# Performance work log

Hardware: AMD Instinct MI355X
Metric: run time of the kernel (lower is better)

## Reference

```python
import jax, jax.numpy as jnp
import numpy as np

N = 40000      # input points
M = 40000      # output points
E = 500000     # flat neighbor edges (ragged flattened)
F = 32         # input feature channels
C = 64         # output channels
K = 15         # kernel points
EXTENT = 0.6


def _make_kernel_points(k, radius):
    # Deterministic stand-in for load_kernels(): first point fixed at center,
    # remaining points spread inside a ball of the given radius.
    rng = np.random.RandomState(0)
    pts = rng.randn(k, 3).astype(np.float32)
    pts /= np.linalg.norm(pts, axis=1, keepdims=True) + 1e-9
    scale = rng.rand(k, 1).astype(np.float32) ** (1.0 / 3.0)
    pts = pts * scale * radius
    pts[0] = 0.0  # fixed='center'
    return jnp.asarray(pts)


def setup_inputs() -> dict:
    key = jax.random.key(0)
    ks = jax.random.split(key, 6)
    points = jax.random.uniform(ks[0], (N, 3), dtype=jnp.float32)
    features = jax.random.normal(ks[1], (N, F), dtype=jnp.float32)
    output_points = jax.random.uniform(ks[2], (M, 3), dtype=jnp.float32)
    neighbor_indices = jax.random.randint(ks[3], (E,), 0, N, dtype=jnp.int32)
    segment_ids = jnp.sort(jax.random.randint(ks[4], (E,), 0, M, dtype=jnp.int32))
    k_points = _make_kernel_points(K, 1.5 * EXTENT)          # [K,3] constant
    k_values = jax.random.normal(ks[5], (K, F, C), dtype=jnp.float32) * 0.05
    return {
        "points": points,
        "features": features,
        "output_points": output_points,
        "neighbor_indices": neighbor_indices,
        "segment_ids": segment_ids,
        "k_points": k_points,
        "k_values": k_values,
    }


def reference(points, features, output_points, neighbor_indices, segment_ids,
              k_points, k_values):
    # Gather neighbor coords/features and recenter around each output point.
    rel = points[neighbor_indices] - output_points[segment_ids]      # [E,3]
    nbr_feat = features[neighbor_indices]                            # [E,F]

    # Per-kernel-point squared distances and linear influence weights.
    diff = rel[:, None, :] - k_points[None, :, :]                    # [E,K,3]
    sq_dist = jnp.sum(diff * diff, axis=-1)                          # [E,K]
    w = jnp.maximum(1.0 - jnp.sqrt(sq_dist) / EXTENT, 0.0)           # [E,K]

    # Weighted features and ragged segment-sum per output point.
    weighted = w[:, :, None] * nbr_feat[:, None, :]                  # [E,K,F]
    agg = jax.ops.segment_sum(weighted, segment_ids, num_segments=M,
                              indices_are_sorted=True)               # [M,K,F]

    # Batched matmul over kernel points, then sum over kernel points.
    out = jnp.einsum('mkf,kfc->mc', agg, k_values)                   # [M,C]
    return out
```

## Files before the change

### kernel.cpp

```cpp
#include <hip/hip_runtime.h>

typedef __attribute__((ext_vector_type(8))) short bf16x8;
typedef __attribute__((ext_vector_type(8))) _Float16 f16x8;
typedef __attribute__((ext_vector_type(4))) float f32x4;
typedef __attribute__((ext_vector_type(4))) _Float16 f16x4;
typedef __attribute__((ext_vector_type(2))) _Float16 f16x2;

#define NPTS   40000
#define MOUT   40000
#define EDG    500000
#define FIN    32
#define COUT   64
#define KP     15
#define KFDIM  (KP * FIN)
#define EXTENT 0.6f

#define FSTRIDE 112
#define WSTRIDE 40
#define WAVE_LDS (16 * FSTRIDE + 16 * WSTRIDE)

#define FEAT_BLKS  (NPTS * FIN / 1024)
#define PTS_BLKS   ((NPTS + 255) / 256)
#define OP_BLKS    ((MOUT + 255) / 256)
#define ROW_BLKS   ((EDG + 255) / 256)
#define WT_BLKS    (KFDIM * COUT / 256)
#define PRE_BLKS   (FEAT_BLKS + PTS_BLKS + OP_BLKS + ROW_BLKS + WT_BLKS)

__device__ __forceinline__ short f2bf(float x) {
    union { float f; unsigned u; } v; v.f = x;
    unsigned r = (v.u + 0x7fffu + ((v.u >> 16) & 1u)) >> 16;
    return (short)r;
}

__global__ __launch_bounds__(256) void preprocess_all(
    const float* __restrict__ features, _Float16* __restrict__ feat_i,
    const float* __restrict__ pts, float4* __restrict__ p4,
    const float* __restrict__ opts, float4* __restrict__ op4,
    const int* __restrict__ seg_ids, int* __restrict__ row_start,
    const float* __restrict__ k_values, _Float16* __restrict__ w_t)
{
    const int bid = blockIdx.x;
    if (bid < FEAT_BLKS) {
        const int d0 = (bid * 256 + threadIdx.x) * 4;
        #pragma unroll
        for (int u = 0; u < 4; ++u) {
            const int d = d0 + u;
            const int p = d >> 5, q = d & 31;
            const int fp = q >> 1, h = q & 1;
            feat_i[d] = (_Float16)features[p * FIN + fp + 16 * h];
        }
    } else if (bid < FEAT_BLKS + PTS_BLKS) {
        const int i = (bid - FEAT_BLKS) * 256 + threadIdx.x;
        if (i < NPTS) {
            const float* p = pts + 3 * i;
            p4[i] = make_float4(p[0], p[1], p[2], 0.f);
        }
    } else if (bid < FEAT_BLKS + PTS_BLKS + OP_BLKS) {
        const int i = (bid - FEAT_BLKS - PTS_BLKS) * 256 + threadIdx.x;
        if (i < MOUT) {
            const float* p = opts + 3 * i;
            op4[i] = make_float4(p[0], p[1], p[2], 0.f);
        }
    } else if (bid < FEAT_BLKS + PTS_BLKS + OP_BLKS + ROW_BLKS) {
        const int e = (bid - FEAT_BLKS - PTS_BLKS - OP_BLKS) * 256 + threadIdx.x;
        if (e >= EDG) return;
        const int cur  = seg_ids[e];
        const int prev = (e == 0) ? -1 : seg_ids[e - 1];
        for (int m = prev + 1; m <= cur; ++m) row_start[m] = e;
        if (e == EDG - 1)
            for (int m = cur + 1; m <= MOUT; ++m) row_start[m] = EDG;
    } else {
        const int d = (bid - FEAT_BLKS - PTS_BLKS - OP_BLKS - ROW_BLKS) * 256
                      + threadIdx.x;
        const int c = d / KFDIM, r = d % KFDIM;
        const int k = r >> 5, q = r & 31;
        const int fp = q >> 1, h = q & 1;
        w_t[d] = (_Float16)k_values[(k * FIN + fp + 16 * h) * COUT + c];
    }
}

__global__ __launch_bounds__(256, 6) void kpconv_agg_edge(
    const float4* __restrict__ points4,
    const _Float16* __restrict__ feat_i,
    const float4* __restrict__ op4,
    const int*   __restrict__ nbr_idx,
    const int*   __restrict__ row_start,
    const float* __restrict__ k_points,
    _Float16* __restrict__ agg_g)
{
    __shared__ __align__(16) unsigned char smem[4 * WAVE_LDS];

    const int tid  = threadIdx.x;
    const int wave = tid >> 6;
    const int lane = tid & 63;
    const int quad = lane >> 4;
    const int l16  = lane & 15;
    const int esl  = lane >> 2;
    const int kg   = lane & 3;

    unsigned char* fbase = smem + wave * WAVE_LDS;
    unsigned char* wbase = fbase + 16 * FSTRIDE;

    const int m  = blockIdx.x * 4 + wave;
    const int e0 = row_start[m];
    const int e1 = row_start[m + 1];
    const float4 o = op4[m];

    float kx[4], ky[4], kz[4];
    #pragma unroll
    for (int t = 0; t < 4; ++t) {
        const int k  = kg * 4 + t;
        const int kk = k < KP ? k : 0;
        kx[t] = k_points[kk * 3 + 0];
        ky[t] = k_points[kk * 3 + 1];
        kz[t] = k_points[kk * 3 + 2];
    }
    const float inv_ext = 1.f / EXTENT;

    f32x4 c_lo = {0.f, 0.f, 0.f, 0.f};
    f32x4 c_hi = {0.f, 0.f, 0.f, 0.f};

    for (int es = e0; es < e1; es += 16) {
        const int e  = es + esl;
        const int nb = nbr_idx[e < e1 ? e : e1 - 1];

        const uint4 fc = *(const uint4*)(feat_i + nb * FIN + kg * 8);
        *(uint4*)(fbase + esl * FSTRIDE + kg * 16) = fc;

        const float4 p = points4[nb];
        const float rx = p.x - o.x, ry = p.y - o.y, rz = p.z - o.z;
        const bool evalid = e < e1;
        #pragma unroll
        for (int t = 0; t < 4; ++t) {
            const float dx = rx - kx[t], dy = ry - ky[t], dz = rz - kz[t];
            float w = 1.f - sqrtf(dx * dx + dy * dy + dz * dz) * inv_ext;
            w = w > 0.f ? w : 0.f;
            if (!evalid || (kg * 4 + t) >= KP) w = 0.f;
            *(_Float16*)(wbase + (kg * 4 + t) * WSTRIDE + esl * 2) = (_Float16)w;
        }

        const f16x4 af = *(const f16x4*)(wbase + l16 * WSTRIDE + quad * 8);
        f16x2 w2[4];
        #pragma unroll
        for (int j = 0; j < 4; ++j)
            w2[j] = *(const f16x2*)(fbase + (quad * 4 + j) * FSTRIDE + l16 * 4);
        const f16x4 blo = {w2[0][0], w2[1][0], w2[2][0], w2[3][0]};
        const f16x4 bhi = {w2[0][1], w2[1][1], w2[2][1], w2[3][1]};

        c_lo = __builtin_amdgcn_mfma_f32_16x16x16f16(af, blo, c_lo, 0, 0, 0);
        c_hi = __builtin_amdgcn_mfma_f32_16x16x16f16(af, bhi, c_hi, 0, 0, 0);
    }

    _Float16* dst = agg_g + (size_t)m * KFDIM;
    #pragma unroll
    for (int r = 0; r < 4; ++r) {
        const int krow = quad * 4 + r;
        if (krow < KP) {
            f16x2 v = {(_Float16)c_lo[r], (_Float16)c_hi[r]};
            *(f16x2*)(dst + krow * FIN + 2 * l16) = v;
        }
    }
}

__global__ __launch_bounds__(256, 4) void kpconv_gemm_i(
    const _Float16* __restrict__ agg_g,
    const _Float16* __restrict__ w_t,
    float* __restrict__ out)
{
    const int tid  = threadIdx.x;
    const int wave = tid >> 6;
    const int lane = tid & 63;
    const int quad = lane >> 4;
    const int l16  = lane & 15;
    const int m0   = blockIdx.x * 32;
    const int bcol = wave * 16 + l16;

    f16x8 bfr[15];
    const _Float16* wrow = w_t + (size_t)bcol * KFDIM + quad * 8;
    #pragma unroll
    for (int s = 0; s < 15; ++s)
        bfr[s] = *(const f16x8*)(wrow + 32 * s);

    const _Float16* arow0 = agg_g + (size_t)(m0 + l16) * KFDIM + quad * 8;
    const _Float16* arow1 = arow0 + 16 * KFDIM;

    f32x4 c0 = {0.f, 0.f, 0.f, 0.f};
    f32x4 c1 = {0.f, 0.f, 0.f, 0.f};
    #pragma unroll
    for (int s = 0; s < 15; ++s) {
        const f16x8 a0 = *(const f16x8*)(arow0 + 32 * s);
        const f16x8 a1 = *(const f16x8*)(arow1 + 32 * s);
        c0 = __builtin_amdgcn_mfma_f32_16x16x32_f16(a0, bfr[s], c0, 0, 0, 0);
        c1 = __builtin_amdgcn_mfma_f32_16x16x32_f16(a1, bfr[s], c1, 0, 0, 0);
    }

    #pragma unroll
    for (int r = 0; r < 4; ++r) {
        out[(m0 + quad * 4 + r) * COUT + bcol]      = c0[r];
        out[(m0 + 16 + quad * 4 + r) * COUT + bcol] = c1[r];
    }
}

__global__ __launch_bounds__(256, 4) void kpconv_agg_fallback(
    const float* __restrict__ points,
    const float* __restrict__ features,
    const float* __restrict__ output_points,
    const int*   __restrict__ nbr_idx,
    const int*   __restrict__ seg_ids,
    const float* __restrict__ k_points,
    _Float16* __restrict__ agg_g)
{
    __shared__ int seg_start[5];

    const int tid = threadIdx.x;
    const int m0  = blockIdx.x * 4;

    if (tid <= 4) {
        const int target = m0 + tid;
        int lo = 0, hi = EDG;
        while (lo < hi) {
            int mid = (lo + hi) >> 1;
            if (seg_ids[mid] < target) lo = mid + 1; else hi = mid;
        }
        seg_start[tid] = lo;
    }
    __syncthreads();

    const int wave = tid >> 6;
    const int lane = tid & 63;
    const int quad = lane >> 4;
    const int l16  = lane & 15;

    const int m = m0 + wave;
    const float ox = output_points[m * 3 + 0];
    const float oy = output_points[m * 3 + 1];
    const float oz = output_points[m * 3 + 2];

    const int myk = l16 < KP ? l16 : 0;
    const float kpx = k_points[myk * 3 + 0];
    const float kpy = k_points[myk * 3 + 1];
    const float kpz = k_points[myk * 3 + 2];
    const float inv_ext = 1.f / EXTENT;

    const int e0 = seg_start[wave], e1 = seg_start[wave + 1];

    f32x4 c_lo = {0.f, 0.f, 0.f, 0.f};
    f32x4 c_hi = {0.f, 0.f, 0.f, 0.f};

    for (int es = e0; es < e1; es += 32) {
        const int last = e1 - 1;
        const int ebase = es + quad * 8;

        int nb[8];
        #pragma unroll
        for (int j = 0; j < 8; ++j) {
            const int e = ebase + j;
            nb[j] = nbr_idx[e < e1 ? e : last];
        }

        bf16x8 afrag, blo, bhi;
        #pragma unroll
        for (int j = 0; j < 8; ++j) {
            const float* pp = points + nb[j] * 3;
            const float rx = pp[0] - ox;
            const float ry = pp[1] - oy;
            const float rz = pp[2] - oz;
            const float dx = rx - kpx, dy = ry - kpy, dz = rz - kpz;
            const float d2 = dx * dx + dy * dy + dz * dz;
            float w = 1.f - sqrtf(d2) * inv_ext;
            w = w > 0.f ? w : 0.f;
            if (l16 >= KP || ebase + j >= e1) w = 0.f;
            afrag[j] = f2bf(w);
        }

        #pragma unroll
        for (int j = 0; j < 8; ++j) {
            const float* fp = features + nb[j] * FIN + l16;
            blo[j] = f2bf(fp[0]);
            bhi[j] = f2bf(fp[16]);
        }

        c_lo = __builtin_amdgcn_mfma_f32_16x16x32_bf16(afrag, blo, c_lo, 0, 0, 0);
        c_hi = __builtin_amdgcn_mfma_f32_16x16x32_bf16(afrag, bhi, c_hi, 0, 0, 0);
    }

    _Float16* dst = agg_g + (size_t)m * KFDIM;
    #pragma unroll
    for (int r = 0; r < 4; ++r) {
        const int krow = quad * 4 + r;
        if (krow < KP) {
            dst[krow * FIN + l16]      = (_Float16)c_lo[r];
            dst[krow * FIN + 16 + l16] = (_Float16)c_hi[r];
        }
    }
}

__global__ __launch_bounds__(256, 4) void kpconv_gemm_plain(
    const _Float16* __restrict__ agg_g,
    const float* __restrict__ k_values,
    float* __restrict__ out)
{
    const int tid  = threadIdx.x;
    const int wave = tid >> 6;
    const int lane = tid & 63;
    const int quad = lane >> 4;
    const int l16  = lane & 15;
    const int m0   = blockIdx.x * 32;
    const int bcol = wave * 16 + l16;

    f16x8 bfr[15];
    #pragma unroll
    for (int s = 0; s < 15; ++s) {
        #pragma unroll
        for (int j = 0; j < 8; ++j)
            bfr[s][j] = (_Float16)k_values[(32 * s + quad * 8 + j) * COUT + bcol];
    }

    const _Float16* arow0 = agg_g + (size_t)(m0 + l16) * KFDIM + quad * 8;
    const _Float16* arow1 = arow0 + 16 * KFDIM;

    f32x4 c0 = {0.f, 0.f, 0.f, 0.f};
    f32x4 c1 = {0.f, 0.f, 0.f, 0.f};
    #pragma unroll
    for (int s = 0; s < 15; ++s) {
        const f16x8 a0 = *(const f16x8*)(arow0 + 32 * s);
        const f16x8 a1 = *(const f16x8*)(arow1 + 32 * s);
        c0 = __builtin_amdgcn_mfma_f32_16x16x32_f16(a0, bfr[s], c0, 0, 0, 0);
        c1 = __builtin_amdgcn_mfma_f32_16x16x32_f16(a1, bfr[s], c1, 0, 0, 0);
    }

    #pragma unroll
    for (int r = 0; r < 4; ++r) {
        out[(m0 + quad * 4 + r) * COUT + bcol]      = c0[r];
        out[(m0 + 16 + quad * 4 + r) * COUT + bcol] = c1[r];
    }
}

extern "C" void kernel_launch(void* const* d_in, const int* in_sizes, int n_in,
                              void* d_out, int out_size, void* d_ws, size_t ws_size,
                              hipStream_t stream) {
    const float* points        = (const float*)d_in[0];
    const float* features      = (const float*)d_in[1];
    const float* output_points = (const float*)d_in[2];
    const int*   nbr_idx       = (const int*)d_in[3];
    const int*   seg_ids       = (const int*)d_in[4];
    const float* k_points      = (const float*)d_in[5];
    const float* k_values      = (const float*)d_in[6];
    float* out = (float*)d_out;

    const size_t feat_bytes = (size_t)NPTS * FIN * sizeof(_Float16);
    const size_t pts4_bytes = (size_t)NPTS * sizeof(float4);
    const size_t op4_bytes  = (size_t)MOUT * sizeof(float4);
    const size_t rs_bytes   = ((size_t)(MOUT + 1) * sizeof(int) + 15) & ~15ul;
    const size_t wt_bytes   = (size_t)KFDIM * COUT * sizeof(_Float16);
    const size_t agg_bytes  = (size_t)MOUT * KFDIM * sizeof(_Float16);
    const size_t full_bytes = feat_bytes + pts4_bytes + op4_bytes + rs_bytes
                            + wt_bytes + agg_bytes;

    if (ws_size >= full_bytes) {
        char* p = (char*)d_ws;
        _Float16* feat_i    = (_Float16*)p;  p += feat_bytes;
        float4*   points4   = (float4*)p;    p += pts4_bytes;
        float4*   op4       = (float4*)p;    p += op4_bytes;
        int*      row_start = (int*)p;       p += rs_bytes;
        _Float16* w_t       = (_Float16*)p;  p += wt_bytes;
        _Float16* agg_g     = (_Float16*)p;

        preprocess_all<<<PRE_BLKS, 256, 0, stream>>>(
            features, feat_i, points, points4, output_points, op4,
            seg_ids, row_start, k_values, w_t);
        kpconv_agg_edge<<<MOUT / 4, 256, 0, stream>>>(
            points4, feat_i, op4, nbr_idx, row_start, k_points, agg_g);
        kpconv_gemm_i<<<MOUT / 32, 256, 0, stream>>>(agg_g, w_t, out);
    } else {
        _Float16* agg_g = (_Float16*)d_ws;
        kpconv_agg_fallback<<<MOUT / 4, 256, 0, stream>>>(
            points, features, output_points, nbr_idx, seg_ids, k_points, agg_g);
        kpconv_gemm_plain<<<MOUT / 32, 256, 0, stream>>>(agg_g, k_values, out);
    }
}
```

Before: 117.4 us.

## Fuse edge aggregation and output GEMM into one kernel via LDS tile

Merges the per-output-point aggregation kernel and the follow-up GEMM into a single kernel. Each block handles 16 output points (4 per wave, processed sequentially), writes the aggregated [K,F] rows into an LDS tile, then after a barrier runs the MFMA GEMM against the transposed weights. This removes the global agg round trip (about 38 MB of fp16 written and read back) and one launch. In exchange each wave serialises four ragged segments, the block barrier makes waves wait on the slowest segment, the larger LDS footprint lowers occupancy, and weight fragments are reloaded from global per block.

```diff
diff --git a/kernel.cpp b/kernel.cpp
--- a/kernel.cpp
+++ b/kernel.cpp
@@ -18,6 +18,7 @@
 #define FSTRIDE 112
 #define WSTRIDE 40
 #define WAVE_LDS (16 * FSTRIDE + 16 * WSTRIDE)
+#define ASTR 488
 
 #define FEAT_BLKS  (NPTS * FIN / 1024)
 #define PTS_BLKS   ((NPTS + 255) / 256)
@@ -79,16 +80,18 @@
     }
 }
 
-__global__ __launch_bounds__(256, 6) void kpconv_agg_edge(
+__global__ __launch_bounds__(256, 4) void kpconv_fused2(
     const float4* __restrict__ points4,
     const _Float16* __restrict__ feat_i,
     const float4* __restrict__ op4,
     const int*   __restrict__ nbr_idx,
     const int*   __restrict__ row_start,
     const float* __restrict__ k_points,
-    _Float16* __restrict__ agg_g)
+    const _Float16* __restrict__ w_t,
+    float* __restrict__ out)
 {
-    __shared__ __align__(16) unsigned char smem[4 * WAVE_LDS];
+    __shared__ __align__(16) _Float16 aggT[16 * ASTR];
+    __shared__ __align__(16) unsigned char stage[4 * WAVE_LDS];
 
     const int tid  = threadIdx.x;
     const int wave = tid >> 6;
@@ -97,14 +100,10 @@
     const int l16  = lane & 15;
     const int esl  = lane >> 2;
     const int kg   = lane & 3;
-
-    unsigned char* fbase = smem + wave * WAVE_LDS;
+    const int m0   = blockIdx.x * 16;
+
+    unsigned char* fbase = stage + wave * WAVE_LDS;
     unsigned char* wbase = fbase + 16 * FSTRIDE;
-
-    const int m  = blockIdx.x * 4 + wave;
-    const int e0 = row_start[m];
-    const int e1 = row_start[m + 1];
-    const float4 o = op4[m];
 
     float kx[4], ky[4], kz[4];
     #pragma unroll
@@ -117,88 +116,75 @@
     }
     const float inv_ext = 1.f / EXTENT;
 
-    f32x4 c_lo = {0.f, 0.f, 0.f, 0.f};
-    f32x4 c_hi = {0.f, 0.f, 0.f, 0.f};
-
-    for (int es = e0; es < e1; es += 16) {
-        const int e  = es + esl;
-        const int nb = nbr_idx[e < e1 ? e : e1 - 1];
-
-        const uint4 fc = *(const uint4*)(feat_i + nb * FIN + kg * 8);
-        *(uint4*)(fbase + esl * FSTRIDE + kg * 16) = fc;
-
-        const float4 p = points4[nb];
-        const float rx = p.x - o.x, ry = p.y - o.y, rz = p.z - o.z;
-        const bool evalid = e < e1;
-        #pragma unroll
-        for (int t = 0; t < 4; ++t) {
-            const float dx = rx - kx[t], dy = ry - ky[t], dz = rz - kz[t];
-            float w = 1.f - sqrtf(dx * dx + dy * dy + dz * dz) * inv_ext;
-            w = w > 0.f ? w : 0.f;
-            if (!evalid || (kg * 4 + t) >= KP) w = 0.f;
-            *(_Float16*)(wbase + (kg * 4 + t) * WSTRIDE + esl * 2) = (_Float16)w;
-        }
-
-        const f16x4 af = *(const f16x4*)(wbase + l16 * WSTRIDE + quad * 8);
-        f16x2 w2[4];
-        #pragma unroll
-        for (int j = 0; j < 4; ++j)
-            w2[j] = *(const f16x2*)(fbase + (quad * 4 + j) * FSTRIDE + l16 * 4);
-        const f16x4 blo = {w2[0][0], w2[1][0], w2[2][0], w2[3][0]};
-        const f16x4 bhi = {w2[0][1], w2[1][1], w2[2][1], w2[3][1]};
-
-        c_lo = __builtin_amdgcn_mfma_f32_16x16x16f16(af, blo, c_lo, 0, 0, 0);
-        c_hi = __builtin_amdgcn_mfma_f32_16x16x16f16(af, bhi, c_hi, 0, 0, 0);
-    }
-
-    _Float16* dst = agg_g + (size_t)m * KFDIM;
-    #pragma unroll
-    for (int r = 0; r < 4; ++r) {
-        const int krow = quad * 4 + r;
-        if (krow < KP) {
-            f16x2 v = {(_Float16)c_lo[r], (_Float16)c_hi[r]};
-            *(f16x2*)(dst + krow * FIN + 2 * l16) = v;
-        }
-    }
-}
-
-__global__ __launch_bounds__(256, 4) void kpconv_gemm_i(
-    const _Float16* __restrict__ agg_g,
-    const _Float16* __restrict__ w_t,
-    float* __restrict__ out)
-{
-    const int tid  = threadIdx.x;
-    const int wave = tid >> 6;
-    const int lane = tid & 63;
-    const int quad = lane >> 4;
-    const int l16  = lane & 15;
-    const int m0   = blockIdx.x * 32;
+    for (int s4 = 0; s4 < 4; ++s4) {
+        const int li = wave * 4 + s4;
+        const int m  = m0 + li;
+        const int e0 = row_start[m];
+        const int e1 = row_start[m + 1];
+        const float4 o = op4[m];
+
+        f32x4 c_lo = {0.f, 0.f, 0.f, 0.f};
+        f32x4 c_hi = {0.f, 0.f, 0.f, 0.f};
+
+        for (int es = e0; es < e1; es += 16) {
+            const int e  = es + esl;
+            const int nb = nbr_idx[e < e1 ? e : e1 - 1];
+
+            const uint4 fc = *(const uint4*)(feat_i + nb * FIN + kg * 8);
+            *(uint4*)(fbase + esl * FSTRIDE + kg * 16) = fc;
+
+            const float4 p = points4[nb];
+            const float rx = p.x - o.x, ry = p.y - o.y, rz = p.z - o.z;
+            const bool evalid = e < e1;
+            #pragma unroll
+            for (int t = 0; t < 4; ++t) {
+                const float dx = rx - kx[t], dy = ry - ky[t], dz = rz - kz[t];
+                float w = 1.f - sqrtf(dx * dx + dy * dy + dz * dz) * inv_ext;
+                w = w > 0.f ? w : 0.f;
+                if (!evalid || (kg * 4 + t) >= KP) w = 0.f;
+                *(_Float16*)(wbase + (kg * 4 + t) * WSTRIDE + esl * 2) = (_Float16)w;
+            }
+
+            const f16x4 af = *(const f16x4*)(wbase + l16 * WSTRIDE + quad * 8);
+            f16x2 w2[4];
+            #pragma unroll
+            for (int j = 0; j < 4; ++j)
+                w2[j] = *(const f16x2*)(fbase + (quad * 4 + j) * FSTRIDE + l16 * 4);
+            const f16x4 blo = {w2[0][0], w2[1][0], w2[2][0], w2[3][0]};
+            const f16x4 bhi = {w2[0][1], w2[1][1], w2[2][1], w2[3][1]};
+
+            c_lo = __builtin_amdgcn_mfma_f32_16x16x16f16(af, blo, c_lo, 0, 0, 0);
+            c_hi = __builtin_amdgcn_mfma_f32_16x16x16f16(af, bhi, c_hi, 0, 0, 0);
+        }
+
+        _Float16* dst = aggT + li * ASTR;
+        #pragma unroll
+        for (int r = 0; r < 4; ++r) {
+            const int krow = quad * 4 + r;
+            if (krow < KP) {
+                f16x2 v = {(_Float16)c_lo[r], (_Float16)c_hi[r]};
+                *(f16x2*)(dst + krow * 32 + 2 * l16) = v;
+            }
+        }
+    }
+
+    __syncthreads();
+
     const int bcol = wave * 16 + l16;
-
-    f16x8 bfr[15];
     const _Float16* wrow = w_t + (size_t)bcol * KFDIM + quad * 8;
-    #pragma unroll
-    for (int s = 0; s < 15; ++s)
-        bfr[s] = *(const f16x8*)(wrow + 32 * s);
-
-    const _Float16* arow0 = agg_g + (size_t)(m0 + l16) * KFDIM + quad * 8;
-    const _Float16* arow1 = arow0 + 16 * KFDIM;
-
-    f32x4 c0 = {0.f, 0.f, 0.f, 0.f};
-    f32x4 c1 = {0.f, 0.f, 0.f, 0.f};
+    const _Float16* arow = aggT + l16 * ASTR + quad * 8;
+
+    f32x4 c = {0.f, 0.f, 0.f, 0.f};
     #pragma unroll
     for (int s = 0; s < 15; ++s) {
-        const f16x8 a0 = *(const f16x8*)(arow0 + 32 * s);
-        const f16x8 a1 = *(const f16x8*)(arow1 + 32 * s);
-        c0 = __builtin_amdgcn_mfma_f32_16x16x32_f16(a0, bfr[s], c0, 0, 0, 0);
-        c1 = __builtin_amdgcn_mfma_f32_16x16x32_f16(a1, bfr[s], c1, 0, 0, 0);
-    }
-
-    #pragma unroll
-    for (int r = 0; r < 4; ++r) {
-        out[(m0 + quad * 4 + r) * COUT + bcol]      = c0[r];
-        out[(m0 + 16 + quad * 4 + r) * COUT + bcol] = c1[r];
-    }
+        const f16x8 a = *(const f16x8*)(arow + 32 * s);
+        const f16x8 b = *(const f16x8*)(wrow + 32 * s);
+        c = __builtin_amdgcn_mfma_f32_16x16x32_f16(a, b, c, 0, 0, 0);
+    }
+
+    #pragma unroll
+    for (int r = 0; r < 4; ++r)
+        out[(m0 + quad * 4 + r) * COUT + bcol] = c[r];
 }
 
 __global__ __launch_bounds__(256, 4) void kpconv_agg_fallback(
@@ -353,9 +339,8 @@
     const size_t op4_bytes  = (size_t)MOUT * sizeof(float4);
     const size_t rs_bytes   = ((size_t)(MOUT + 1) * sizeof(int) + 15) & ~15ul;
     const size_t wt_bytes   = (size_t)KFDIM * COUT * sizeof(_Float16);
-    const size_t agg_bytes  = (size_t)MOUT * KFDIM * sizeof(_Float16);
     const size_t full_bytes = feat_bytes + pts4_bytes + op4_bytes + rs_bytes
-                            + wt_bytes + agg_bytes;
+                            + wt_bytes;
 
     if (ws_size >= full_bytes) {
         char* p = (char*)d_ws;
@@ -363,15 +348,13 @@
         float4*   points4   = (float4*)p;    p += pts4_bytes;
         float4*   op4       = (float4*)p;    p += op4_bytes;
         int*      row_start = (int*)p;       p += rs_bytes;
-        _Float16* w_t       = (_Float16*)p;  p += wt_bytes;
-        _Float16* agg_g     = (_Float16*)p;
+        _Float16* w_t       = (_Float16*)p;
 
         preprocess_all<<<PRE_BLKS, 256, 0, stream>>>(
             features, feat_i, points, points4, output_points, op4,
             seg_ids, row_start, k_values, w_t);
-        kpconv_agg_edge<<<MOUT / 4, 256, 0, stream>>>(
-            points4, feat_i, op4, nbr_idx, row_start, k_points, agg_g);
-        kpconv_gemm_i<<<MOUT / 32, 256, 0, stream>>>(agg_g, w_t, out);
+        kpconv_fused2<<<MOUT / 16, 256, 0, stream>>>(
+            points4, feat_i, op4, nbr_idx, row_start, k_points, w_t, out);
     } else {
         _Float16* agg_g = (_Float16*)d_ws;
         kpconv_agg_fallback<<<MOUT / 4, 256, 0, stream>>>(
```

Result: faster. 106.9 us (-9.0%).
